# Performance work log

Measured on AMD Instinct MI355X. Metric: run time of the kernel, lower is better.

## Reference

```python
import jax, jax.numpy as jnp
import numpy as np
import math

NUM_FREQS = 10
DK = 5
TRADEOFF = 1.0  # euclidean_cosine_tradeoff


def posenc(x, L=NUM_FREQS):
    # NeRF positional encoding without identity: [..., D] -> [..., L*2*D]
    freqs = (2.0 ** jnp.arange(L)).astype(x.dtype)          # [L]
    xb = x[..., None, :] * freqs[:, None]                    # [..., L, D]
    enc = jnp.stack([jnp.sin(xb), jnp.cos(xb)], axis=-2)     # [..., L, 2, D]
    return enc.reshape(x.shape[:-1] + (L * 2 * x.shape[-1],))


def setup_inputs() -> dict:
    key = jax.random.key(0)
    k = jax.random.split(key, 6)
    N, C, E = 500000, 64, 3 * 2 * NUM_FREQS  # 500k points, 64 clusters, embed 60
    X = jax.random.normal(k[0], (N, 3), dtype=jnp.float32)
    cluster_ids = jax.random.randint(k[1], (N,), 0, C)
    linear_mappings = jax.random.normal(k[2], (C * 3, E), dtype=jnp.float32) * 0.1
    # xavier-uniform-like init for Wq/Wk
    lim = math.sqrt(6.0 / (E + DK))
    Wq = jax.random.uniform(k[3], (DK, E), dtype=jnp.float32, minval=-lim, maxval=lim)
    Wk = jax.random.uniform(k[4], (DK, E), dtype=jnp.float32, minval=-lim, maxval=lim)
    Wv = jnp.eye(3, dtype=jnp.float32)  # module sets Wv.weight = eye(3)
    centroids = jax.random.normal(k[5], (C, 3), dtype=jnp.float32)
    return {"X": X, "cluster_ids": cluster_ids, "linear_mappings": linear_mappings,
            "Wq": Wq, "Wk": Wk, "Wv": Wv, "centroids": centroids}


def reference(X, cluster_ids, linear_mappings, Wq, Wk, Wv, centroids):
    N = X.shape[0]
    enc = posenc(X)                                           # [N, 60]
    rgb_clusters = (enc @ linear_mappings.T).reshape(N, -1, 3)  # [N, C, 3]
    # kmeans_rgb = rgb_clusters[arange(N), cluster_ids]
    kmeans_rgb = jnp.take_along_axis(
        rgb_clusters, cluster_ids[:, None, None], axis=1)[:, 0]  # [N, 3]
    # self-attention over clusters
    Q = enc[:, :3 * 2 * NUM_FREQS] @ Wq.T                     # [N, dk]
    K = posenc(centroids) @ Wk.T                              # [C, dk]
    V = rgb_clusters @ Wv.T                                   # [N, C, dv]
    scores = (Q @ K.T) / jnp.asarray(math.sqrt(DK), enc.dtype)  # [N, C]
    attn = jax.nn.softmax(scores, axis=-1)
    # original: per-chunk (attn @ V) then diagonal == per-row weighted sum
    attention_rgb = jnp.einsum('nc,ncd->nd', attn, V)         # [N, 3]
    out = kmeans_rgb * TRADEOFF + attention_rgb * (1.0 - TRADEOFF)
    return out, kmeans_rgb, attention_rgb
```

## Files before the change

kernel.cpp:

```cpp
#include <hip/hip_runtime.h>
#include <math.h>

#define NUM_FREQS 10
#define EDIM 60
#define KPAD 64
#define TRADEOFF 1.0f

typedef __attribute__((ext_vector_type(8))) short bf16x8;
typedef __attribute__((ext_vector_type(4))) float f32x4;

__device__ __forceinline__ unsigned short f2bf(float f) {
    unsigned u = __builtin_bit_cast(unsigned, f);
    u += 0x7FFFu + ((u >> 16) & 1u);
    return (unsigned short)(u >> 16);
}

__device__ __forceinline__ float swz16(float x) {
    return __builtin_bit_cast(float,
        __builtin_amdgcn_ds_swizzle(__builtin_bit_cast(int, x), 0x401F));
}

__device__ __forceinline__ void posenc3_fast(float x0, float x1, float x2, float* enc) {
    float xs[3] = {x0, x1, x2};
#pragma unroll
    for (int d = 0; d < 3; ++d) {
        float s, c;
        sincosf(xs[d], &s, &c);
        enc[0*6 + d] = s; enc[0*6 + 3 + d] = c;
#pragma unroll
        for (int l = 1; l < NUM_FREQS; ++l) {
            float s2 = 2.0f * s * c;
            float c2 = 1.0f - 2.0f * s * s;
            s = s2; c = c2;
            enc[l*6 + d] = s; enc[l*6 + 3 + d] = c;
        }
    }
}

__global__ __launch_bounds__(256) void fused1(
        const float* __restrict__ X,
        const int*   __restrict__ cluster_ids,
        const float* __restrict__ lm,
        const float* __restrict__ Wq,
        const float* __restrict__ Wk,
        const float* __restrict__ Wv,
        const float* __restrict__ cents,
        float* __restrict__ out,
        int N) {
    __shared__ __align__(16) unsigned short sA[256 * KPAD];
    __shared__ __align__(16) float sParts[2][16][68];
    __shared__ __align__(16) float sKm[2][16][4];
    __shared__ float sKq[64][5];
    __shared__ int   sCid[256];

    const int tid  = threadIdx.x;
    const int lane = tid & 63;
    const int w    = tid >> 6;
    const int g    = lane >> 4;
    const int l15  = lane & 15;
    const int base = blockIdx.x * 256;

    {
        int n = base + tid; if (n >= N) n = N - 1;
        sCid[tid] = cluster_ids[n];
        float enc[KPAD];
        posenc3_fast(X[n*3+0], X[n*3+1], X[n*3+2], enc);
        enc[60] = 0.f; enc[61] = 0.f; enc[62] = 0.f; enc[63] = 0.f;
#pragma unroll
        for (int u8 = 0; u8 < 8; ++u8) {
            const int slot = u8 ^ (tid & 7);
            bf16x8 v;
#pragma unroll
            for (int j = 0; j < 8; ++j) v[j] = (short)f2bf(enc[u8*8 + j]);
            *(bf16x8*)&sA[tid*KPAD + slot*8] = v;
        }
    }

    {
        const int c = 16*w + l15;
        float enc[EDIM];
        posenc3_fast(cents[c*3+0], cents[c*3+1], cents[c*3+2], enc);
        const float isd = 0.4472135954999579f;
        const f32x4* wk4 = (const f32x4*)(Wk + g*EDIM);
        float a = 0.f;
#pragma unroll
        for (int q = 0; q < 15; ++q) {
            f32x4 v = wk4[q];
            a = fmaf(enc[q*4+0], v[0], a); a = fmaf(enc[q*4+1], v[1], a);
            a = fmaf(enc[q*4+2], v[2], a); a = fmaf(enc[q*4+3], v[3], a);
        }
        sKq[c][g] = a * isd;
        if (g == 0) {
            const f32x4* wk4b = (const f32x4*)(Wk + 4*EDIM);
            float b = 0.f;
#pragma unroll
            for (int q = 0; q < 15; ++q) {
                f32x4 v = wk4b[q];
                b = fmaf(enc[q*4+0], v[0], b); b = fmaf(enc[q*4+1], v[1], b);
                b = fmaf(enc[q*4+2], v[2], b); b = fmaf(enc[q*4+3], v[3], b);
            }
            sKq[c][4] = b * isd;
        }
    }

    bf16x8 afr[4][2];
#pragma unroll
    for (int t = 0; t < 3; ++t) {
        const float* rp = lm + (3*(16*w + l15) + t) * EDIM;
#pragma unroll
        for (int kf = 0; kf < 2; ++kf) {
            const int k0 = (kf*4 + g) * 8;
            float v[8];
            f32x4 p0 = *(const f32x4*)(rp + k0);
            v[0]=p0[0]; v[1]=p0[1]; v[2]=p0[2]; v[3]=p0[3];
            if (k0 + 4 < EDIM) {
                f32x4 p1 = *(const f32x4*)(rp + k0 + 4);
                v[4]=p1[0]; v[5]=p1[1]; v[6]=p1[2]; v[7]=p1[3];
            } else { v[4]=0.f; v[5]=0.f; v[6]=0.f; v[7]=0.f; }
            bf16x8 pk;
#pragma unroll
            for (int j = 0; j < 8; ++j) pk[j] = (short)f2bf(v[j]);
            afr[t][kf] = pk;
        }
    }

    const float wv00 = Wv[0], wv01 = Wv[1], wv02 = Wv[2];
    const float wv10 = Wv[3], wv11 = Wv[4], wv12 = Wv[5];
    const float wv20 = Wv[6], wv21 = Wv[7], wv22 = Wv[8];

    __syncthreads();

    {
        const int c = 16*w + l15;
        const float kq0 = sKq[c][0], kq1 = sKq[c][1], kq2 = sKq[c][2],
                    kq3 = sKq[c][3], kq4 = sKq[c][4];
#pragma unroll
        for (int kf = 0; kf < 2; ++kf) {
            const int k0 = (kf*4 + g) * 8;
            bf16x8 pk;
#pragma unroll
            for (int j = 0; j < 8; ++j) {
                const int k = k0 + j;
                float a = 0.f;
                if (k < EDIM)
                    a = Wq[0*EDIM+k]*kq0 + Wq[1*EDIM+k]*kq1 + Wq[2*EDIM+k]*kq2
                      + Wq[3*EDIM+k]*kq3 + Wq[4*EDIM+k]*kq4;
                pk[j] = (short)f2bf(a);
            }
            afr[3][kf] = pk;
        }
    }

    float* o_out = out;
    float* o_km  = out + (size_t)N * 3;
    float* o_at  = out + (size_t)N * 6;

    for (int s = 0; s < 16; ++s) {
        bf16x8 bfr[2];
        const int prow = s*16 + l15;
#pragma unroll
        for (int kf = 0; kf < 2; ++kf) {
            const int slot = (kf*4 + g) ^ (prow & 7);
            bfr[kf] = *(const bf16x8*)&sA[prow*KPAD + slot*8];
        }
        f32x4 acc[4];
#pragma unroll
        for (int t = 0; t < 4; ++t) {
            acc[t] = (f32x4){0.f, 0.f, 0.f, 0.f};
#pragma unroll
            for (int kf = 0; kf < 2; ++kf)
                acc[t] = __builtin_amdgcn_mfma_f32_16x16x32_bf16(afr[t][kf], bfr[kf], acc[t], 0, 0, 0);
        }

        const int cid = sCid[s*16 + l15];
        const int cbase = 16*w + 4*g;

        const float sc0 = acc[3][0], sc1 = acc[3][1], sc2 = acc[3][2], sc3 = acc[3][3];
        const float m4 = fmaxf(fmaxf(sc0, sc1), fmaxf(sc2, sc3));
        const float m8 = fmaxf(m4, swz16(m4));

        const float e0 = __expf(sc0 - m8), e1 = __expf(sc1 - m8),
                    e2 = __expf(sc2 - m8), e3 = __expf(sc3 - m8);
        const float S4 = e0 + e1 + e2 + e3;
        const float a04 = e0*acc[0][0] + e1*acc[0][1] + e2*acc[0][2] + e3*acc[0][3];
        const float a14 = e0*acc[1][0] + e1*acc[1][1] + e2*acc[1][2] + e3*acc[1][3];
        const float a24 = e0*acc[2][0] + e1*acc[2][1] + e2*acc[2][2] + e3*acc[2][3];

        const float S8 = S4  + swz16(S4);
        const float a0 = a04 + swz16(a04);
        const float a1 = a14 + swz16(a14);
        const float a2 = a24 + swz16(a24);

#pragma unroll
        for (int rg = 0; rg < 4; ++rg) {
            if (cbase + rg == cid) {
                *(f32x4*)&sKm[s & 1][l15][0] =
                    (f32x4){acc[0][rg], acc[1][rg], acc[2][rg], 0.f};
            }
        }

        if (!(g & 1)) {
            const int grp = w*2 + (g >> 1);
            float* pp = &sParts[s & 1][l15][grp*8];
            *(f32x4*)pp = (f32x4){m8, S8, a0, a1};
            pp[4] = a2;
        }

        if (s > 0 && w == ((s - 1) & 3) && lane < 16) {
            const int sp = s - 1;
            const int n = base + sp*16 + lane;
            float mi[8], Si[8], A0[8], A1[8], A2[8];
            float mg = -INFINITY;
#pragma unroll
            for (int i = 0; i < 8; ++i) {
                const float* pp = &sParts[sp & 1][lane][i*8];
                f32x4 v = *(const f32x4*)pp;
                mi[i] = v[0]; Si[i] = v[1]; A0[i] = v[2]; A1[i] = v[3]; A2[i] = pp[4];
                mg = fmaxf(mg, mi[i]);
            }
            float S = 0.f, t0 = 0.f, t1 = 0.f, t2 = 0.f;
#pragma unroll
            for (int i = 0; i < 8; ++i) {
                const float f = __expf(mi[i] - mg);
                S  = fmaf(Si[i], f, S);
                t0 = fmaf(A0[i], f, t0); t1 = fmaf(A1[i], f, t1); t2 = fmaf(A2[i], f, t2);
            }
            const f32x4 km = *(const f32x4*)&sKm[sp & 1][lane][0];
            const float inv = 1.0f / S;
            const float u0 = t0*inv, u1 = t1*inv, u2 = t2*inv;
            const float at0 = wv00*u0 + wv01*u1 + wv02*u2;
            const float at1 = wv10*u0 + wv11*u1 + wv12*u2;
            const float at2 = wv20*u0 + wv21*u1 + wv22*u2;
            if (n < N) {
                const float oo0 = km[0]*TRADEOFF + at0*(1.0f - TRADEOFF);
                const float oo1 = km[1]*TRADEOFF + at1*(1.0f - TRADEOFF);
                const float oo2 = km[2]*TRADEOFF + at2*(1.0f - TRADEOFF);
                o_out[n*3+0] = oo0;   o_out[n*3+1] = oo1;   o_out[n*3+2] = oo2;
                o_km[n*3+0]  = km[0]; o_km[n*3+1]  = km[1]; o_km[n*3+2]  = km[2];
                o_at[n*3+0]  = at0;   o_at[n*3+1]  = at1;   o_at[n*3+2]  = at2;
            }
        }
        __syncthreads();
    }

    if (w == 3 && lane < 16) {
        const int sp = 15;
        const int n = base + sp*16 + lane;
        float mi[8], Si[8], A0[8], A1[8], A2[8];
        float mg = -INFINITY;
#pragma unroll
        for (int i = 0; i < 8; ++i) {
            const float* pp = &sParts[sp & 1][lane][i*8];
            f32x4 v = *(const f32x4*)pp;
            mi[i] = v[0]; Si[i] = v[1]; A0[i] = v[2]; A1[i] = v[3]; A2[i] = pp[4];
            mg = fmaxf(mg, mi[i]);
        }
        float S = 0.f, t0 = 0.f, t1 = 0.f, t2 = 0.f;
#pragma unroll
        for (int i = 0; i < 8; ++i) {
            const float f = __expf(mi[i] - mg);
            S  = fmaf(Si[i], f, S);
            t0 = fmaf(A0[i], f, t0); t1 = fmaf(A1[i], f, t1); t2 = fmaf(A2[i], f, t2);
        }
        const f32x4 km = *(const f32x4*)&sKm[sp & 1][lane][0];
        const float inv = 1.0f / S;
        const float u0 = t0*inv, u1 = t1*inv, u2 = t2*inv;
        const float at0 = wv00*u0 + wv01*u1 + wv02*u2;
        const float at1 = wv10*u0 + wv11*u1 + wv12*u2;
        const float at2 = wv20*u0 + wv21*u1 + wv22*u2;
        if (n < N) {
            const float oo0 = km[0]*TRADEOFF + at0*(1.0f - TRADEOFF);
            const float oo1 = km[1]*TRADEOFF + at1*(1.0f - TRADEOFF);
            const float oo2 = km[2]*TRADEOFF + at2*(1.0f - TRADEOFF);
            o_out[n*3+0] = oo0;   o_out[n*3+1] = oo1;   o_out[n*3+2] = oo2;
            o_km[n*3+0]  = km[0]; o_km[n*3+1]  = km[1]; o_km[n*3+2]  = km[2];
            o_at[n*3+0]  = at0;   o_at[n*3+1]  = at1;   o_at[n*3+2]  = at2;
        }
    }
}

extern "C" void kernel_launch(void* const* d_in, const int* in_sizes, int n_in,
                              void* d_out, int out_size, void* d_ws, size_t ws_size,
                              hipStream_t stream) {
    const float* X         = (const float*)d_in[0];
    const int*   cids      = (const int*)  d_in[1];
    const float* lm        = (const float*)d_in[2];
    const float* Wq        = (const float*)d_in[3];
    const float* Wk        = (const float*)d_in[4];
    const float* Wv        = (const float*)d_in[5];
    const float* centroids = (const float*)d_in[6];
    float* out = (float*)d_out;
    const int N = in_sizes[0] / 3;

    const int blocks = (N + 255) / 256;
    fused1<<<blocks, 256, 0, stream>>>(X, cids, lm, Wq, Wk, Wv, centroids, out, N);
}
```

Measured before the change: 133.0 us.

## Make fused kernel persistent and use hardware sin/cos for positional encoding

Converts the kernel to a persistent grid-stride loop over 256-point chunks with a grid capped at 768 blocks. Per-block setup (centroid key projection, bf16 conversion of linear mappings and the Q·K fold) is amortized across many chunks instead of being redone for each of ~1954 blocks. Positional encoding now uses fract plus hardware sin/cos per frequency instead of sincosf followed by double-angle recurrence, and bf16 conversion uses the native cast. This trades some accuracy at high frequencies and adds an extra barrier per chunk.

```diff
diff --git a/kernel.cpp b/kernel.cpp
--- a/kernel.cpp
+++ b/kernel.cpp
@@ -9,10 +9,8 @@
 typedef __attribute__((ext_vector_type(8))) short bf16x8;
 typedef __attribute__((ext_vector_type(4))) float f32x4;
 
-__device__ __forceinline__ unsigned short f2bf(float f) {
-    unsigned u = __builtin_bit_cast(unsigned, f);
-    u += 0x7FFFu + ((u >> 16) & 1u);
-    return (unsigned short)(u >> 16);
+__device__ __forceinline__ short bfc(float f) {
+    return __builtin_bit_cast(short, (__bf16)f);
 }
 
 __device__ __forceinline__ float swz16(float x) {
@@ -20,24 +18,23 @@
         __builtin_amdgcn_ds_swizzle(__builtin_bit_cast(int, x), 0x401F));
 }
 
-__device__ __forceinline__ void posenc3_fast(float x0, float x1, float x2, float* enc) {
+__device__ __forceinline__ void posenc3(float x0, float x1, float x2, float* enc) {
+    const float inv2pi = 0.15915494309189535f;
     float xs[3] = {x0, x1, x2};
 #pragma unroll
     for (int d = 0; d < 3; ++d) {
-        float s, c;
-        sincosf(xs[d], &s, &c);
-        enc[0*6 + d] = s; enc[0*6 + 3 + d] = c;
-#pragma unroll
-        for (int l = 1; l < NUM_FREQS; ++l) {
-            float s2 = 2.0f * s * c;
-            float c2 = 1.0f - 2.0f * s * s;
-            s = s2; c = c2;
-            enc[l*6 + d] = s; enc[l*6 + 3 + d] = c;
-        }
-    }
-}
-
-__global__ __launch_bounds__(256) void fused1(
+        float xr = xs[d] * inv2pi;
+#pragma unroll
+        for (int l = 0; l < NUM_FREQS; ++l) {
+            const float fr = __builtin_amdgcn_fractf(xr);
+            enc[l*6 + d]     = __builtin_amdgcn_sinf(fr);
+            enc[l*6 + 3 + d] = __builtin_amdgcn_cosf(fr);
+            xr *= 2.0f;
+        }
+    }
+}
+
+__global__ __launch_bounds__(256) void fused2(
         const float* __restrict__ X,
         const int*   __restrict__ cluster_ids,
         const float* __restrict__ lm,
@@ -46,7 +43,7 @@
         const float* __restrict__ Wv,
         const float* __restrict__ cents,
         float* __restrict__ out,
-        int N) {
+        int N, int nChunks) {
     __shared__ __align__(16) unsigned short sA[256 * KPAD];
     __shared__ __align__(16) float sParts[2][16][68];
     __shared__ __align__(16) float sKm[2][16][4];
@@ -58,28 +55,11 @@
     const int w    = tid >> 6;
     const int g    = lane >> 4;
     const int l15  = lane & 15;
-    const int base = blockIdx.x * 256;
-
-    {
-        int n = base + tid; if (n >= N) n = N - 1;
-        sCid[tid] = cluster_ids[n];
-        float enc[KPAD];
-        posenc3_fast(X[n*3+0], X[n*3+1], X[n*3+2], enc);
-        enc[60] = 0.f; enc[61] = 0.f; enc[62] = 0.f; enc[63] = 0.f;
-#pragma unroll
-        for (int u8 = 0; u8 < 8; ++u8) {
-            const int slot = u8 ^ (tid & 7);
-            bf16x8 v;
-#pragma unroll
-            for (int j = 0; j < 8; ++j) v[j] = (short)f2bf(enc[u8*8 + j]);
-            *(bf16x8*)&sA[tid*KPAD + slot*8] = v;
-        }
-    }
 
     {
         const int c = 16*w + l15;
         float enc[EDIM];
-        posenc3_fast(cents[c*3+0], cents[c*3+1], cents[c*3+2], enc);
+        posenc3(cents[c*3+0], cents[c*3+1], cents[c*3+2], enc);
         const float isd = 0.4472135954999579f;
         const f32x4* wk4 = (const f32x4*)(Wk + g*EDIM);
         float a = 0.f;
@@ -119,7 +99,7 @@
             } else { v[4]=0.f; v[5]=0.f; v[6]=0.f; v[7]=0.f; }
             bf16x8 pk;
 #pragma unroll
-            for (int j = 0; j < 8; ++j) pk[j] = (short)f2bf(v[j]);
+            for (int j = 0; j < 8; ++j) pk[j] = bfc(v[j]);
             afr[t][kf] = pk;
         }
     }
@@ -145,7 +125,7 @@
                 if (k < EDIM)
                     a = Wq[0*EDIM+k]*kq0 + Wq[1*EDIM+k]*kq1 + Wq[2*EDIM+k]*kq2
                       + Wq[3*EDIM+k]*kq3 + Wq[4*EDIM+k]*kq4;
-                pk[j] = (short)f2bf(a);
+                pk[j] = bfc(a);
             }
             afr[3][kf] = pk;
         }
@@ -155,59 +135,118 @@
     float* o_km  = out + (size_t)N * 3;
     float* o_at  = out + (size_t)N * 6;
 
-    for (int s = 0; s < 16; ++s) {
-        bf16x8 bfr[2];
-        const int prow = s*16 + l15;
-#pragma unroll
-        for (int kf = 0; kf < 2; ++kf) {
-            const int slot = (kf*4 + g) ^ (prow & 7);
-            bfr[kf] = *(const bf16x8*)&sA[prow*KPAD + slot*8];
-        }
-        f32x4 acc[4];
-#pragma unroll
-        for (int t = 0; t < 4; ++t) {
-            acc[t] = (f32x4){0.f, 0.f, 0.f, 0.f};
-#pragma unroll
-            for (int kf = 0; kf < 2; ++kf)
-                acc[t] = __builtin_amdgcn_mfma_f32_16x16x32_bf16(afr[t][kf], bfr[kf], acc[t], 0, 0, 0);
-        }
-
-        const int cid = sCid[s*16 + l15];
-        const int cbase = 16*w + 4*g;
-
-        const float sc0 = acc[3][0], sc1 = acc[3][1], sc2 = acc[3][2], sc3 = acc[3][3];
-        const float m4 = fmaxf(fmaxf(sc0, sc1), fmaxf(sc2, sc3));
-        const float m8 = fmaxf(m4, swz16(m4));
-
-        const float e0 = __expf(sc0 - m8), e1 = __expf(sc1 - m8),
-                    e2 = __expf(sc2 - m8), e3 = __expf(sc3 - m8);
-        const float S4 = e0 + e1 + e2 + e3;
-        const float a04 = e0*acc[0][0] + e1*acc[0][1] + e2*acc[0][2] + e3*acc[0][3];
-        const float a14 = e0*acc[1][0] + e1*acc[1][1] + e2*acc[1][2] + e3*acc[1][3];
-        const float a24 = e0*acc[2][0] + e1*acc[2][1] + e2*acc[2][2] + e3*acc[2][3];
-
-        const float S8 = S4  + swz16(S4);
-        const float a0 = a04 + swz16(a04);
-        const float a1 = a14 + swz16(a14);
-        const float a2 = a24 + swz16(a24);
-
-#pragma unroll
-        for (int rg = 0; rg < 4; ++rg) {
-            if (cbase + rg == cid) {
-                *(f32x4*)&sKm[s & 1][l15][0] =
-                    (f32x4){acc[0][rg], acc[1][rg], acc[2][rg], 0.f};
-            }
-        }
-
-        if (!(g & 1)) {
-            const int grp = w*2 + (g >> 1);
-            float* pp = &sParts[s & 1][l15][grp*8];
-            *(f32x4*)pp = (f32x4){m8, S8, a0, a1};
-            pp[4] = a2;
-        }
-
-        if (s > 0 && w == ((s - 1) & 3) && lane < 16) {
-            const int sp = s - 1;
+    for (int chunk = blockIdx.x; chunk < nChunks; chunk += gridDim.x) {
+        const int base = chunk << 8;
+
+        __syncthreads();
+
+        {
+            int n = base + tid; if (n >= N) n = N - 1;
+            sCid[tid] = cluster_ids[n];
+            float enc[KPAD];
+            posenc3(X[n*3+0], X[n*3+1], X[n*3+2], enc);
+            enc[60] = 0.f; enc[61] = 0.f; enc[62] = 0.f; enc[63] = 0.f;
+#pragma unroll
+            for (int u8 = 0; u8 < 8; ++u8) {
+                const int slot = u8 ^ (tid & 7);
+                bf16x8 v;
+#pragma unroll
+                for (int j = 0; j < 8; ++j) v[j] = bfc(enc[u8*8 + j]);
+                *(bf16x8*)&sA[tid*KPAD + slot*8] = v;
+            }
+        }
+        __syncthreads();
+
+        for (int s = 0; s < 16; ++s) {
+            bf16x8 bfr[2];
+            const int prow = s*16 + l15;
+#pragma unroll
+            for (int kf = 0; kf < 2; ++kf) {
+                const int slot = (kf*4 + g) ^ (prow & 7);
+                bfr[kf] = *(const bf16x8*)&sA[prow*KPAD + slot*8];
+            }
+            f32x4 acc[4];
+#pragma unroll
+            for (int t = 0; t < 4; ++t) {
+                acc[t] = (f32x4){0.f, 0.f, 0.f, 0.f};
+#pragma unroll
+                for (int kf = 0; kf < 2; ++kf)
+                    acc[t] = __builtin_amdgcn_mfma_f32_16x16x32_bf16(afr[t][kf], bfr[kf], acc[t], 0, 0, 0);
+            }
+
+            const int cid = sCid[s*16 + l15];
+            const int cbase = 16*w + 4*g;
+
+            const float sc0 = acc[3][0], sc1 = acc[3][1], sc2 = acc[3][2], sc3 = acc[3][3];
+            const float m4 = fmaxf(fmaxf(sc0, sc1), fmaxf(sc2, sc3));
+            const float m8 = fmaxf(m4, swz16(m4));
+
+            const float e0 = __expf(sc0 - m8), e1 = __expf(sc1 - m8),
+                        e2 = __expf(sc2 - m8), e3 = __expf(sc3 - m8);
+            const float S4  = (e0 + e1) + (e2 + e3);
+            const float a04 = fmaf(e0, acc[0][0], fmaf(e1, acc[0][1], fmaf(e2, acc[0][2], e3*acc[0][3])));
+            const float a14 = fmaf(e0, acc[1][0], fmaf(e1, acc[1][1], fmaf(e2, acc[1][2], e3*acc[1][3])));
+            const float a24 = fmaf(e0, acc[2][0], fmaf(e1, acc[2][1], fmaf(e2, acc[2][2], e3*acc[2][3])));
+
+            const float S8 = S4  + swz16(S4);
+            const float a0 = a04 + swz16(a04);
+            const float a1 = a14 + swz16(a14);
+            const float a2 = a24 + swz16(a24);
+
+#pragma unroll
+            for (int rg = 0; rg < 4; ++rg) {
+                if (cbase + rg == cid) {
+                    *(f32x4*)&sKm[s & 1][l15][0] =
+                        (f32x4){acc[0][rg], acc[1][rg], acc[2][rg], 0.f};
+                }
+            }
+
+            if (!(g & 1)) {
+                const int grp = w*2 + (g >> 1);
+                float* pp = &sParts[s & 1][l15][grp*8];
+                *(f32x4*)pp = (f32x4){m8, S8, a0, a1};
+                pp[4] = a2;
+            }
+
+            if (s > 0 && w == ((s - 1) & 3) && lane < 16) {
+                const int sp = s - 1;
+                const int n = base + sp*16 + lane;
+                float mi[8], Si[8], A0[8], A1[8], A2[8];
+                float mg = -INFINITY;
+#pragma unroll
+                for (int i = 0; i < 8; ++i) {
+                    const float* pp = &sParts[sp & 1][lane][i*8];
+                    f32x4 v = *(const f32x4*)pp;
+                    mi[i] = v[0]; Si[i] = v[1]; A0[i] = v[2]; A1[i] = v[3]; A2[i] = pp[4];
+                    mg = fmaxf(mg, mi[i]);
+                }
+                float S = 0.f, t0 = 0.f, t1 = 0.f, t2 = 0.f;
+#pragma unroll
+                for (int i = 0; i < 8; ++i) {
+                    const float f = __expf(mi[i] - mg);
+                    S  = fmaf(Si[i], f, S);
+                    t0 = fmaf(A0[i], f, t0); t1 = fmaf(A1[i], f, t1); t2 = fmaf(A2[i], f, t2);
+                }
+                const f32x4 km = *(const f32x4*)&sKm[sp & 1][lane][0];
+                const float inv = 1.0f / S;
+                const float u0 = t0*inv, u1 = t1*inv, u2 = t2*inv;
+                const float at0 = wv00*u0 + wv01*u1 + wv02*u2;
+                const float at1 = wv10*u0 + wv11*u1 + wv12*u2;
+                const float at2 = wv20*u0 + wv21*u1 + wv22*u2;
+                if (n < N) {
+                    const float oo0 = km[0]*TRADEOFF + at0*(1.0f - TRADEOFF);
+                    const float oo1 = km[1]*TRADEOFF + at1*(1.0f - TRADEOFF);
+                    const float oo2 = km[2]*TRADEOFF + at2*(1.0f - TRADEOFF);
+                    o_out[n*3+0] = oo0;   o_out[n*3+1] = oo1;   o_out[n*3+2] = oo2;
+                    o_km[n*3+0]  = km[0]; o_km[n*3+1]  = km[1]; o_km[n*3+2]  = km[2];
+                    o_at[n*3+0]  = at0;   o_at[n*3+1]  = at1;   o_at[n*3+2]  = at2;
+                }
+            }
+            __syncthreads();
+        }
+
+        if (w == 3 && lane < 16) {
+            const int sp = 15;
             const int n = base + sp*16 + lane;
             float mi[8], Si[8], A0[8], A1[8], A2[8];
             float mg = -INFINITY;
@@ -240,42 +279,6 @@
                 o_at[n*3+0]  = at0;   o_at[n*3+1]  = at1;   o_at[n*3+2]  = at2;
             }
         }
-        __syncthreads();
-    }
-
-    if (w == 3 && lane < 16) {
-        const int sp = 15;
-        const int n = base + sp*16 + lane;
-        float mi[8], Si[8], A0[8], A1[8], A2[8];
-        float mg = -INFINITY;
-#pragma unroll
-        for (int i = 0; i < 8; ++i) {
-            const float* pp = &sParts[sp & 1][lane][i*8];
-            f32x4 v = *(const f32x4*)pp;
-            mi[i] = v[0]; Si[i] = v[1]; A0[i] = v[2]; A1[i] = v[3]; A2[i] = pp[4];
-            mg = fmaxf(mg, mi[i]);
-        }
-        float S = 0.f, t0 = 0.f, t1 = 0.f, t2 = 0.f;
-#pragma unroll
-        for (int i = 0; i < 8; ++i) {
-            const float f = __expf(mi[i] - mg);
-            S  = fmaf(Si[i], f, S);
-            t0 = fmaf(A0[i], f, t0); t1 = fmaf(A1[i], f, t1); t2 = fmaf(A2[i], f, t2);
-        }
-        const f32x4 km = *(const f32x4*)&sKm[sp & 1][lane][0];
-        const float inv = 1.0f / S;
-        const float u0 = t0*inv, u1 = t1*inv, u2 = t2*inv;
-        const float at0 = wv00*u0 + wv01*u1 + wv02*u2;
-        const float at1 = wv10*u0 + wv11*u1 + wv12*u2;
-        const float at2 = wv20*u0 + wv21*u1 + wv22*u2;
-        if (n < N) {
-            const float oo0 = km[0]*TRADEOFF + at0*(1.0f - TRADEOFF);
-            const float oo1 = km[1]*TRADEOFF + at1*(1.0f - TRADEOFF);
-            const float oo2 = km[2]*TRADEOFF + at2*(1.0f - TRADEOFF);
-            o_out[n*3+0] = oo0;   o_out[n*3+1] = oo1;   o_out[n*3+2] = oo2;
-            o_km[n*3+0]  = km[0]; o_km[n*3+1]  = km[1]; o_km[n*3+2]  = km[2];
-            o_at[n*3+0]  = at0;   o_at[n*3+1]  = at1;   o_at[n*3+2]  = at2;
-        }
     }
 }
 
@@ -292,6 +295,7 @@
     float* out = (float*)d_out;
     const int N = in_sizes[0] / 3;
 
-    const int blocks = (N + 255) / 256;
-    fused1<<<blocks, 256, 0, stream>>>(X, cids, lm, Wq, Wk, Wv, centroids, out, N);
-}
+    const int nChunks = (N + 255) / 256;
+    const int grid = nChunks < 768 ? nChunks : 768;
+    fused2<<<grid, 256, 0, stream>>>(X, cids, lm, Wq, Wk, Wv, centroids, out, N, nChunks);
+}
```

After: 124.0 us. 1.07x faster.
